# Kernel optimization log

Hardware: AMD Instinct MI355X
Metric: run time of the kernel (lower is better)

Reference implementation:

```python
import jax, jax.numpy as jnp
import numpy as np
import itertools

R_MAX = 0.4
POWER = 0
B, N_ATOMS, K_OPS = 16, 256, 16

# 27 periodic image shifts, same order as itertools.product([0,1,-1], repeat=3)
SHIFTS = jnp.asarray(list(itertools.product([0, 1, -1], repeat=3)), dtype=jnp.float32)  # [27,3]


def _pair_sq_sum(f, r):
    """sum over neighbor pairs (dist<=r) of elementwise (frac_dst-frac_src)**2.

    Equivalent to torch get_neighbors (cdist over 27 shifted copies, radius
    mask, gather) followed by (vec*vec).sum(dim=0), without materializing
    the variable-length edge list. f: [N,3] -> out: [3]."""
    n = f.shape[0]
    # shift-major replication: f_ex[s*n + i] = f[i] + SHIFTS[s], matching
    # torch.cat([frac]*27) + shifts.repeat_interleave(n)
    f_ex = (f[None, :, :] + SHIFTS[:, None, :]).reshape(27 * n, 3)
    d = f_ex[None, :, :] - f[:, None, :]          # [N, 27N, 3] = dst - src
    dist2 = jnp.sum(d * d, axis=-1)               # [N, 27N]
    mask = (jnp.sqrt(dist2) <= r).astype(f.dtype)
    return jnp.einsum('ij,ijc->c', mask, d * d)   # [3]


def setup_inputs() -> dict:
    key = jax.random.key(0)
    k1, k2 = jax.random.split(key)
    fracs = jax.random.uniform(k1, (B * N_ATOMS, 3), dtype=jnp.float32)
    natms = jnp.full((B,), N_ATOMS, dtype=jnp.int32)
    oprss = jax.random.normal(k2, (B * K_OPS, 3, 3), dtype=jnp.float32)
    noprs = jnp.full((B,), K_OPS, dtype=jnp.int32)
    return {"fracs": fracs, "natms": natms, "oprss": oprss, "noprs": noprs}


def reference(fracs, natms, oprss, noprs):
    b = natms.shape[0]
    n = fracs.shape[0] // b          # uniform atoms per structure (static)
    k = oprss.shape[0] // noprs.shape[0]  # uniform operators per structure
    fr = fracs.reshape(b, n, 3)
    ops = oprss.reshape(b, k, 3, 3)
    r = R_MAX / (n ** POWER)

    def per_struct(loss, xs):
        f, opset = xs                        # [N,3], [K,3,3]
        out0 = _pair_sq_sum(f, r)            # identical for every opr

        def per_op(opr):
            f1 = (f @ opr.T) % 1.0
            return jnp.linalg.norm(_pair_sq_sum(f1, r) - out0)

        diffs = jax.vmap(per_op)(opset)      # [K]
        return loss + diffs.sum() / (k * b), None

    loss, _ = jax.lax.scan(per_struct, jnp.float32(0.0), (fr, ops))
    return loss
```

## Files before the change

kernel.cpp:

```cpp
#include <hip/hip_runtime.h>
#include <math.h>


#define NATOMS 256
#define KOPS   16
#define NB     16
#define TASKS_PER_B (KOPS + 1)
#define JSPLIT 4
#define TCHUNK 32

__device__ __forceinline__ float wrap01(float x) {
    float m = fmodf(x, 1.0f);
    if (m < 0.0f) m += 1.0f;
    return m;
}

__global__ __launch_bounds__(256) void pair_kernel(
    const float* __restrict__ fracs,
    const float* __restrict__ oprss,
    float* __restrict__ sums)
{
    const int blk  = blockIdx.x;
    const int task = blk >> 2;
    const int q    = blk & 3;
    const int b    = task / TASKS_PER_B;
    const int t    = task - b * TASKS_PER_B;

    const int i = threadIdx.x;
    const float* f = fracs + (size_t)b * NATOMS * 3;

    __shared__ float4 sf[NATOMS];

    float fx = f[i*3+0], fy = f[i*3+1], fz = f[i*3+2];
    if (t > 0) {
        const float* op = oprss + (size_t)(b * KOPS + (t - 1)) * 9;
        float gx = wrap01(fx*op[0] + fy*op[1] + fz*op[2]);
        float gy = wrap01(fx*op[3] + fy*op[4] + fz*op[5]);
        float gz = wrap01(fx*op[6] + fy*op[7] + fz*op[8]);
        fx = gx; fy = gy; fz = gz;
    }
    sf[i] = make_float4(fx, fy, fz, 0.0f);
    __syncthreads();

    float a0 = 0.f, a1 = 0.f, a2 = 0.f;
    const int tbase = q * TCHUNK + 1;
    #pragma unroll 8
    for (int u = 0; u < TCHUNK; ++u) {
        const int j = (i + tbase + u) & (NATOMS - 1);
        const float4 fj = sf[j];
        float dx = fj.x - fx, dy = fj.y - fy, dz = fj.z - fz;
        float vx = (fj.x - rintf(dx)) - fx;
        float vy = (fj.y - rintf(dy)) - fy;
        float vz = (fj.z - rintf(dz)) - fz;
        float px = vx*vx, py = vy*vy, pz = vz*vz;
        float d2 = px + py + pz;
        float m = (d2 <= 0.4f*0.4f) ? 1.0f : 0.0f;
        a0 = fmaf(px, m, a0);
        a1 = fmaf(py, m, a1);
        a2 = fmaf(pz, m, a2);
    }
    a0 *= 2.0f; a1 *= 2.0f; a2 *= 2.0f;

    if (q == 3) {
        const int j = (i + 128) & (NATOMS - 1);
        const float4 fj = sf[j];
        float dx = fj.x - fx, dy = fj.y - fy, dz = fj.z - fz;
        float vx = (fj.x - rintf(dx)) - fx;
        float vy = (fj.y - rintf(dy)) - fy;
        float vz = (fj.z - rintf(dz)) - fz;
        float px = vx*vx, py = vy*vy, pz = vz*vz;
        float d2 = px + py + pz;
        float m = (d2 <= 0.4f*0.4f) ? 1.0f : 0.0f;
        a0 = fmaf(px, -m, a0);
        a1 = fmaf(py, -m, a1);
        a2 = fmaf(pz, -m, a2);
    }

    for (int off = 32; off >= 1; off >>= 1) {
        a0 += __shfl_xor(a0, off);
        a1 += __shfl_xor(a1, off);
        a2 += __shfl_xor(a2, off);
    }
    __shared__ float part[4][3];
    const int wave = i >> 6;
    if ((i & 63) == 0) { part[wave][0] = a0; part[wave][1] = a1; part[wave][2] = a2; }
    __syncthreads();
    if (i == 0) {
        float* dst = sums + (size_t)blk * 3;
        dst[0] = part[0][0] + part[1][0] + part[2][0] + part[3][0];
        dst[1] = part[0][1] + part[1][1] + part[2][1] + part[3][1];
        dst[2] = part[0][2] + part[1][2] + part[2][2] + part[3][2];
    }
}

__global__ __launch_bounds__(256) void finish_kernel(
    const float* __restrict__ sums, float* __restrict__ out)
{
    const int t = threadIdx.x;
    const int b = t >> 4, k = t & 15;
    const float* s0p = sums + (size_t)((b * TASKS_PER_B + 0)     * JSPLIT) * 3;
    const float* skp = sums + (size_t)((b * TASKS_PER_B + 1 + k) * JSPLIT) * 3;
    float s0x = 0.f, s0y = 0.f, s0z = 0.f;
    float skx = 0.f, sky = 0.f, skz = 0.f;
    #pragma unroll
    for (int qq = 0; qq < JSPLIT; ++qq) {
        s0x += s0p[qq*3+0]; s0y += s0p[qq*3+1]; s0z += s0p[qq*3+2];
        skx += skp[qq*3+0]; sky += skp[qq*3+1]; skz += skp[qq*3+2];
    }
    float d0 = skx - s0x, d1 = sky - s0y, d2 = skz - s0z;
    float v = sqrtf(d0*d0 + d1*d1 + d2*d2);

    for (int off = 32; off >= 1; off >>= 1) v += __shfl_xor(v, off);
    __shared__ float part[4];
    if ((t & 63) == 0) part[t >> 6] = v;
    __syncthreads();
    if (t == 0) out[0] = (part[0] + part[1] + part[2] + part[3]) * (1.0f / 256.0f);
}

extern "C" void kernel_launch(void* const* d_in, const int* in_sizes, int n_in,
                              void* d_out, int out_size, void* d_ws, size_t ws_size,
                              hipStream_t stream) {
    const float* fracs = (const float*)d_in[0];
    const float* oprss = (const float*)d_in[2];
    float* out  = (float*)d_out;
    float* sums = (float*)d_ws;

    const int nblk = NB * TASKS_PER_B * JSPLIT;
    pair_kernel<<<nblk, 256, 0, stream>>>(fracs, oprss, sums);
    finish_kernel<<<1, 256, 0, stream>>>(sums, out);
}
```

Measured before the change: 14.73 us.

## Fuse pair sums and final reduction into one kernel with atomic accumulation

Replaces the two-kernel scheme (separate identity and operator tasks, then a finish kernel) with one kernel. Each 1024-thread block handles one (structure, operator) pair and computes both the original and the transformed pair sums, so the identity sum is recomputed 16 times per structure. The per-block norm is added into the output with atomicAdd after a memset. This removes the second kernel launch and the workspace round trip, at the cost of redundant identity work, float atomic ordering nondeterminism, and an extra memset launch.

```diff
diff --git a/kernel.cpp b/kernel.cpp
--- a/kernel.cpp
+++ b/kernel.cpp
@@ -5,9 +5,6 @@
 #define NATOMS 256
 #define KOPS   16
 #define NB     16
-#define TASKS_PER_B (KOPS + 1)
-#define JSPLIT 4
-#define TCHUNK 32
 
 __device__ __forceinline__ float wrap01(float x) {
     float m = fmodf(x, 1.0f);
@@ -15,106 +12,125 @@
     return m;
 }
 
-__global__ __launch_bounds__(256) void pair_kernel(
+__global__ __launch_bounds__(1024) void sgo_kernel(
     const float* __restrict__ fracs,
     const float* __restrict__ oprss,
-    float* __restrict__ sums)
+    float* __restrict__ out)
 {
-    const int blk  = blockIdx.x;
-    const int task = blk >> 2;
-    const int q    = blk & 3;
-    const int b    = task / TASKS_PER_B;
-    const int t    = task - b * TASKS_PER_B;
+    const int blk = blockIdx.x;
+    const int b   = blk >> 4;
+    const int k   = blk & 15;
+    const int tid = threadIdx.x;
+    const int i   = tid & (NATOMS - 1);
+    const int q   = tid >> 8;
 
-    const int i = threadIdx.x;
     const float* f = fracs + (size_t)b * NATOMS * 3;
 
-    __shared__ float4 sf[NATOMS];
+    __shared__ float4 sfi[NATOMS];
+    __shared__ float4 sfo[NATOMS];
 
-    float fx = f[i*3+0], fy = f[i*3+1], fz = f[i*3+2];
-    if (t > 0) {
-        const float* op = oprss + (size_t)(b * KOPS + (t - 1)) * 9;
+    if (q == 0) {
+        float fx = f[i*3+0], fy = f[i*3+1], fz = f[i*3+2];
+        sfi[i] = make_float4(fx, fy, fz, 0.0f);
+    } else if (q == 1) {
+        float fx = f[i*3+0], fy = f[i*3+1], fz = f[i*3+2];
+        const float* op = oprss + (size_t)(b * KOPS + k) * 9;
         float gx = wrap01(fx*op[0] + fy*op[1] + fz*op[2]);
         float gy = wrap01(fx*op[3] + fy*op[4] + fz*op[5]);
         float gz = wrap01(fx*op[6] + fy*op[7] + fz*op[8]);
-        fx = gx; fy = gy; fz = gz;
+        sfo[i] = make_float4(gx, gy, gz, 0.0f);
     }
-    sf[i] = make_float4(fx, fy, fz, 0.0f);
     __syncthreads();
 
+    const float4 fi4 = sfi[i];
+    const float4 fo4 = sfo[i];
+
     float a0 = 0.f, a1 = 0.f, a2 = 0.f;
-    const int tbase = q * TCHUNK + 1;
+    float c0 = 0.f, c1 = 0.f, c2 = 0.f;
+    const int tbase = q * 32 + 1;
     #pragma unroll 8
-    for (int u = 0; u < TCHUNK; ++u) {
+    for (int u = 0; u < 32; ++u) {
         const int j = (i + tbase + u) & (NATOMS - 1);
-        const float4 fj = sf[j];
-        float dx = fj.x - fx, dy = fj.y - fy, dz = fj.z - fz;
-        float vx = (fj.x - rintf(dx)) - fx;
-        float vy = (fj.y - rintf(dy)) - fy;
-        float vz = (fj.z - rintf(dz)) - fz;
-        float px = vx*vx, py = vy*vy, pz = vz*vz;
-        float d2 = px + py + pz;
-        float m = (d2 <= 0.4f*0.4f) ? 1.0f : 0.0f;
-        a0 = fmaf(px, m, a0);
-        a1 = fmaf(py, m, a1);
-        a2 = fmaf(pz, m, a2);
+        {
+            const float4 fj = sfi[j];
+            float dx = fj.x - fi4.x, dy = fj.y - fi4.y, dz = fj.z - fi4.z;
+            float vx = (fj.x - rintf(dx)) - fi4.x;
+            float vy = (fj.y - rintf(dy)) - fi4.y;
+            float vz = (fj.z - rintf(dz)) - fi4.z;
+            float px = vx*vx, py = vy*vy, pz = vz*vz;
+            float d2 = px + py + pz;
+            float m = (d2 <= 0.4f*0.4f) ? 1.0f : 0.0f;
+            a0 = fmaf(px, m, a0);
+            a1 = fmaf(py, m, a1);
+            a2 = fmaf(pz, m, a2);
+        }
+        {
+            const float4 fj = sfo[j];
+            float dx = fj.x - fo4.x, dy = fj.y - fo4.y, dz = fj.z - fo4.z;
+            float vx = (fj.x - rintf(dx)) - fo4.x;
+            float vy = (fj.y - rintf(dy)) - fo4.y;
+            float vz = (fj.z - rintf(dz)) - fo4.z;
+            float px = vx*vx, py = vy*vy, pz = vz*vz;
+            float d2 = px + py + pz;
+            float m = (d2 <= 0.4f*0.4f) ? 1.0f : 0.0f;
+            c0 = fmaf(px, m, c0);
+            c1 = fmaf(py, m, c1);
+            c2 = fmaf(pz, m, c2);
+        }
     }
     a0 *= 2.0f; a1 *= 2.0f; a2 *= 2.0f;
+    c0 *= 2.0f; c1 *= 2.0f; c2 *= 2.0f;
 
     if (q == 3) {
         const int j = (i + 128) & (NATOMS - 1);
-        const float4 fj = sf[j];
-        float dx = fj.x - fx, dy = fj.y - fy, dz = fj.z - fz;
-        float vx = (fj.x - rintf(dx)) - fx;
-        float vy = (fj.y - rintf(dy)) - fy;
-        float vz = (fj.z - rintf(dz)) - fz;
-        float px = vx*vx, py = vy*vy, pz = vz*vz;
-        float d2 = px + py + pz;
-        float m = (d2 <= 0.4f*0.4f) ? 1.0f : 0.0f;
-        a0 = fmaf(px, -m, a0);
-        a1 = fmaf(py, -m, a1);
-        a2 = fmaf(pz, -m, a2);
+        {
+            const float4 fj = sfi[j];
+            float dx = fj.x - fi4.x, dy = fj.y - fi4.y, dz = fj.z - fi4.z;
+            float vx = (fj.x - rintf(dx)) - fi4.x;
+            float vy = (fj.y - rintf(dy)) - fi4.y;
+            float vz = (fj.z - rintf(dz)) - fi4.z;
+            float px = vx*vx, py = vy*vy, pz = vz*vz;
+            float d2 = px + py + pz;
+            float m = (d2 <= 0.4f*0.4f) ? 1.0f : 0.0f;
+            a0 = fmaf(px, -m, a0);
+            a1 = fmaf(py, -m, a1);
+            a2 = fmaf(pz, -m, a2);
+        }
+        {
+            const float4 fj = sfo[j];
+            float dx = fj.x - fo4.x, dy = fj.y - fo4.y, dz = fj.z - fo4.z;
+            float vx = (fj.x - rintf(dx)) - fo4.x;
+            float vy = (fj.y - rintf(dy)) - fo4.y;
+            float vz = (fj.z - rintf(dz)) - fo4.z;
+            float px = vx*vx, py = vy*vy, pz = vz*vz;
+            float d2 = px + py + pz;
+            float m = (d2 <= 0.4f*0.4f) ? 1.0f : 0.0f;
+            c0 = fmaf(px, -m, c0);
+            c1 = fmaf(py, -m, c1);
+            c2 = fmaf(pz, -m, c2);
+        }
     }
 
+    float d0 = c0 - a0, d1 = c1 - a1, d2 = c2 - a2;
     for (int off = 32; off >= 1; off >>= 1) {
-        a0 += __shfl_xor(a0, off);
-        a1 += __shfl_xor(a1, off);
-        a2 += __shfl_xor(a2, off);
+        d0 += __shfl_xor(d0, off);
+        d1 += __shfl_xor(d1, off);
+        d2 += __shfl_xor(d2, off);
     }
-    __shared__ float part[4][3];
-    const int wave = i >> 6;
-    if ((i & 63) == 0) { part[wave][0] = a0; part[wave][1] = a1; part[wave][2] = a2; }
+    __shared__ float part[16][3];
+    const int wave = tid >> 6;
+    if ((tid & 63) == 0) { part[wave][0] = d0; part[wave][1] = d1; part[wave][2] = d2; }
     __syncthreads();
-    if (i == 0) {
-        float* dst = sums + (size_t)blk * 3;
-        dst[0] = part[0][0] + part[1][0] + part[2][0] + part[3][0];
-        dst[1] = part[0][1] + part[1][1] + part[2][1] + part[3][1];
-        dst[2] = part[0][2] + part[1][2] + part[2][2] + part[3][2];
+
+    if (tid == 0) {
+        float sx = 0.f, sy = 0.f, sz = 0.f;
+        #pragma unroll
+        for (int w = 0; w < 16; ++w) {
+            sx += part[w][0]; sy += part[w][1]; sz += part[w][2];
+        }
+        float v = sqrtf(sx*sx + sy*sy + sz*sz);
+        atomicAdd(out, v * (1.0f / 256.0f));
     }
-}
-
-__global__ __launch_bounds__(256) void finish_kernel(
-    const float* __restrict__ sums, float* __restrict__ out)
-{
-    const int t = threadIdx.x;
-    const int b = t >> 4, k = t & 15;
-    const float* s0p = sums + (size_t)((b * TASKS_PER_B + 0)     * JSPLIT) * 3;
-    const float* skp = sums + (size_t)((b * TASKS_PER_B + 1 + k) * JSPLIT) * 3;
-    float s0x = 0.f, s0y = 0.f, s0z = 0.f;
-    float skx = 0.f, sky = 0.f, skz = 0.f;
-    #pragma unroll
-    for (int qq = 0; qq < JSPLIT; ++qq) {
-        s0x += s0p[qq*3+0]; s0y += s0p[qq*3+1]; s0z += s0p[qq*3+2];
-        skx += skp[qq*3+0]; sky += skp[qq*3+1]; skz += skp[qq*3+2];
-    }
-    float d0 = skx - s0x, d1 = sky - s0y, d2 = skz - s0z;
-    float v = sqrtf(d0*d0 + d1*d1 + d2*d2);
-
-    for (int off = 32; off >= 1; off >>= 1) v += __shfl_xor(v, off);
-    __shared__ float part[4];
-    if ((t & 63) == 0) part[t >> 6] = v;
-    __syncthreads();
-    if (t == 0) out[0] = (part[0] + part[1] + part[2] + part[3]) * (1.0f / 256.0f);
 }
 
 extern "C" void kernel_launch(void* const* d_in, const int* in_sizes, int n_in,
@@ -122,10 +138,8 @@
                               hipStream_t stream) {
     const float* fracs = (const float*)d_in[0];
     const float* oprss = (const float*)d_in[2];
-    float* out  = (float*)d_out;
-    float* sums = (float*)d_ws;
+    float* out = (float*)d_out;
 
-    const int nblk = NB * TASKS_PER_B * JSPLIT;
-    pair_kernel<<<nblk, 256, 0, stream>>>(fracs, oprss, sums);
-    finish_kernel<<<1, 256, 0, stream>>>(sums, out);
+    hipMemsetAsync(out, 0, sizeof(float), stream);
+    sgo_kernel<<<NB * KOPS, 1024, 0, stream>>>(fracs, oprss, out);
 }
```

After: 24.48 us. 66.2% more time.
